# Optimization experiments

Hardware: AMD Instinct MI355X
Metric: run time of the kernel (lower is better)

## Reference

```python
import jax, jax.numpy as jnp
import numpy as np

N_NODES = 100000


def gcn_conv(x, W, b, src, dst, num_nodes):
    """PyG GCNConv: add self-loops, symmetric deg^{-1/2} normalization,
    linear transform, scatter-add aggregation (source -> target), bias."""
    h = x @ W  # [N, out]
    # degree on target nodes, counting the added self-loop (+1)
    deg = jax.ops.segment_sum(jnp.ones_like(dst, dtype=h.dtype), dst,
                              num_segments=num_nodes) + 1.0
    dinv = jax.lax.rsqrt(deg)  # deg >= 1 always
    norm = dinv[src] * dinv[dst]  # [E]
    agg = jax.ops.segment_sum(h[src] * norm[:, None], dst,
                              num_segments=num_nodes)
    # self-loop contribution: norm_ii = dinv[i]^2
    out = agg + h * (dinv * dinv)[:, None]
    return out + b


def setup_inputs() -> dict:
    key = jax.random.key(0)
    ks = jax.random.split(key, 8)
    num_features, hidden, emb = 64, 64, 32
    x = jax.random.normal(ks[0], (N_NODES, num_features), dtype=jnp.float32)
    edge_index = jax.random.randint(ks[1], (2, 1600000), 0, N_NODES, dtype=jnp.int64)
    def glorot(k, shape):
        lim = float(np.sqrt(6.0 / (shape[0] + shape[1])))
        return jax.random.uniform(k, shape, jnp.float32, -lim, lim)
    return {
        "x": x,
        "edge_index": edge_index,
        "W1": glorot(ks[2], (num_features, hidden)),
        "b1": jnp.zeros((hidden,), jnp.float32),
        "W2": glorot(ks[3], (hidden, hidden)),
        "b2": jnp.zeros((hidden,), jnp.float32),
        "Wf": glorot(ks[4], (hidden, emb)),
        "bf": jnp.zeros((emb,), jnp.float32),
    }


def reference(x, edge_index, W1, b1, W2, b2, Wf, bf):
    src, dst = edge_index[0], edge_index[1]
    n = x.shape[0]
    h = gcn_conv(x, W1, b1, src, dst, n)
    h = jax.nn.relu(h)  # dropout is identity in eval mode
    h = gcn_conv(h, W2, b2, src, dst, n)
    h = jax.nn.relu(h)
    return h @ Wf + bf
```

## Files before the change

kernel.cpp:

```cpp
#include <hip/hip_runtime.h>


#define NODE_SHIFT 9
#define NODES_PER_BKT 512
#define K1PAD 208
#define NB_PART 256

__device__ __forceinline__ unsigned short f2bf_rne(float f) {
    unsigned int u = __float_as_uint(f);
    unsigned int r = (u + 0x7FFFu + ((u >> 16) & 1u)) >> 16;
    return (unsigned short)r;
}
__device__ __forceinline__ float bf_lo(unsigned int u) {
    return __uint_as_float(u << 16);
}
__device__ __forceinline__ float bf_hi(unsigned int u) {
    return __uint_as_float(u & 0xFFFF0000u);
}

__global__ __launch_bounds__(256) void coarse_hist_kernel(const int* __restrict__ dst, int E,
                                                          int* __restrict__ bkt_partial,
                                                          int K1, int CHK) {
    __shared__ int lcnt[256];
    const int tid = threadIdx.x;
    const int start = blockIdx.x * CHK;
    const int end = min(E, start + CHK);
    for (int k = tid; k < 256; k += 256) lcnt[k] = 0;
    __syncthreads();
    const int s4 = start >> 2;
    const int e4 = end >> 2;
    for (int i = s4 + tid; i < e4; i += 256) {
        const int4 d = ((const int4*)dst)[i];
        atomicAdd(&lcnt[d.x >> NODE_SHIFT], 1);
        atomicAdd(&lcnt[d.y >> NODE_SHIFT], 1);
        atomicAdd(&lcnt[d.z >> NODE_SHIFT], 1);
        atomicAdd(&lcnt[d.w >> NODE_SHIFT], 1);
    }
    __syncthreads();
    for (int k = tid; k < K1; k += 256)
        bkt_partial[blockIdx.x * K1PAD + k] = lcnt[k];
}

__global__ __launch_bounds__(256) void bucket_scan_kernel(const int* __restrict__ bkt_partial,
                                                          int* __restrict__ bkt_start,
                                                          int* __restrict__ bkt_cursor,
                                                          int K1, int E) {
    __shared__ int wsum[4];
    const int tid = threadIdx.x;
    const int lane = tid & 63;
    const int wave = tid >> 6;
    int c = 0;
    if (tid < K1)
        for (int b = 0; b < NB_PART; b++) c += bkt_partial[b * K1PAD + tid];
    int inc = c;
#pragma unroll
    for (int o = 1; o < 64; o <<= 1) {
        int t = __shfl_up(inc, o, 64);
        if (lane >= o) inc += t;
    }
    if (lane == 63) wsum[wave] = inc;
    __syncthreads();
    int wpre = 0;
#pragma unroll
    for (int w = 0; w < 4; w++) wpre += (w < wave) ? wsum[w] : 0;
    const int p = wpre + inc - c;
    if (tid < K1) { bkt_start[tid] = p; bkt_cursor[tid] = p; }
    if (tid == 0) bkt_start[K1] = E;
}

__global__ __launch_bounds__(256) void partition_kernel(const int* __restrict__ src,
                                                        const int* __restrict__ dst, int E,
                                                        int* __restrict__ bkt_cursor,
                                                        int2* __restrict__ staging,
                                                        int K1, int CHK) {
    __shared__ int lcnt[256];
    __shared__ int lcur[256];
    const int tid = threadIdx.x;
    const int start = blockIdx.x * CHK;
    const int end = min(E, start + CHK);
    for (int k = tid; k < 256; k += 256) lcnt[k] = 0;
    __syncthreads();
    const int s4 = start >> 2;
    const int e4 = end >> 2;
    for (int i = s4 + tid; i < e4; i += 256) {
        const int4 d = ((const int4*)dst)[i];
        atomicAdd(&lcnt[d.x >> NODE_SHIFT], 1);
        atomicAdd(&lcnt[d.y >> NODE_SHIFT], 1);
        atomicAdd(&lcnt[d.z >> NODE_SHIFT], 1);
        atomicAdd(&lcnt[d.w >> NODE_SHIFT], 1);
    }
    __syncthreads();
    for (int k = tid; k < K1; k += 256) {
        int cc = lcnt[k];
        lcur[k] = cc ? atomicAdd(&bkt_cursor[k], cc) : 0;
    }
    __syncthreads();
    for (int i = s4 + tid; i < e4; i += 256) {
        const int4 d = ((const int4*)dst)[i];
        const int4 s = ((const int4*)src)[i];
        int pos;
        pos = atomicAdd(&lcur[d.x >> NODE_SHIFT], 1); staging[pos] = make_int2(d.x, s.x);
        pos = atomicAdd(&lcur[d.y >> NODE_SHIFT], 1); staging[pos] = make_int2(d.y, s.y);
        pos = atomicAdd(&lcur[d.z >> NODE_SHIFT], 1); staging[pos] = make_int2(d.z, s.z);
        pos = atomicAdd(&lcur[d.w >> NODE_SHIFT], 1); staging[pos] = make_int2(d.w, s.w);
    }
}

__global__ __launch_bounds__(512) void bucket_build_kernel(const int2* __restrict__ staging,
                                                           const int* __restrict__ bkt_start,
                                                           float* __restrict__ dinv,
                                                           int* __restrict__ offs,
                                                           int* __restrict__ csr_src,
                                                           int N, int E) {
    __shared__ int cnt[NODES_PER_BKT];
    __shared__ int wsum[8];
    const int tid = threadIdx.x;
    const int node0 = blockIdx.x * NODES_PER_BKT;
    const int estart = bkt_start[blockIdx.x];
    const int eend = bkt_start[blockIdx.x + 1];

    cnt[tid] = 0;
    __syncthreads();
    for (int e = estart + tid; e < eend; e += 512)
        atomicAdd(&cnt[staging[e].x - node0], 1);
    __syncthreads();

    const int lane = tid & 63;
    const int wave = tid >> 6;
    const int c = cnt[tid];
    int inc = c;
#pragma unroll
    for (int o = 1; o < 64; o <<= 1) {
        int t = __shfl_up(inc, o, 64);
        if (lane >= o) inc += t;
    }
    if (lane == 63) wsum[wave] = inc;
    __syncthreads();
    int wpre = 0;
#pragma unroll
    for (int w = 0; w < 8; w++) wpre += (w < wave) ? wsum[w] : 0;
    const int p = estart + wpre + inc - c;

    const int node = node0 + tid;
    __syncthreads();
    if (node < N) {
        offs[node] = p;
        dinv[node] = rsqrtf((float)c + 1.0f);
    }
    cnt[tid] = p;
    __syncthreads();
    for (int e = estart + tid; e < eend; e += 512) {
        int2 r = staging[e];
        int pos = atomicAdd(&cnt[r.x - node0], 1);
        csr_src[pos] = r.y;
    }
    if (blockIdx.x == 0 && tid == 0) offs[N] = E;
}

template <int OUTC, int RPT, bool BIAS, bool SCALE, bool BF16OUT>
__global__ __launch_bounds__(256) void gemm_kernel(const float* __restrict__ X,
                                                   const float* __restrict__ W,
                                                   const float* __restrict__ bias,
                                                   const float* __restrict__ dinv,
                                                   void* __restrict__ Yv, int N) {
    constexpr int CG = OUTC / 4;
    constexpr int RG = 256 / CG;
    constexpr int R = RG * RPT;
    constexpr int RPAD = R + (R / 32) * 4;
    __shared__ float Ws[64 * OUTC];
    __shared__ float Xt[64 * RPAD];

    const int tid = threadIdx.x;
    const int row0 = blockIdx.x * R;

    for (int l = tid; l < 64 * OUTC / 4; l += 256)
        ((float4*)Ws)[l] = ((const float4*)W)[l];

    for (int l = tid; l < R * 16; l += 256) {
        const int r = l & (R - 1);
        const int kq = l >> 7;
        float4 v = make_float4(0.f, 0.f, 0.f, 0.f);
        const int row = row0 + r;
        if (row < N) v = ((const float4*)(X + (long)row * 64))[kq];
        const int rp = r + (r >> 5) * 4;
        Xt[(4 * kq + 0) * RPAD + rp] = v.x;
        Xt[(4 * kq + 1) * RPAD + rp] = v.y;
        Xt[(4 * kq + 2) * RPAD + rp] = v.z;
        Xt[(4 * kq + 3) * RPAD + rp] = v.w;
    }
    __syncthreads();

    const int cg = tid % CG;
    const int rg = tid / CG;
    const int c0 = cg * 4;
    const int r0 = rg * RPT;
    const int r0p = r0 + (r0 >> 5) * 4;

    float acc[RPT][4];
#pragma unroll
    for (int i = 0; i < RPT; i++)
#pragma unroll
        for (int j = 0; j < 4; j++) acc[i][j] = 0.f;

#pragma unroll 4
    for (int k = 0; k < 64; k++) {
        float xv[RPT];
        const float4 xa = *(const float4*)&Xt[k * RPAD + r0p];
        xv[0] = xa.x; xv[1] = xa.y; xv[2] = xa.z; xv[3] = xa.w;
        if (RPT == 8) {
            const float4 xb = *(const float4*)&Xt[k * RPAD + r0p + 4];
            xv[4] = xb.x; xv[5] = xb.y; xv[6] = xb.z; xv[7] = xb.w;
        }
        const float4 wa = *(const float4*)&Ws[k * OUTC + c0];
        const float wv[4] = {wa.x, wa.y, wa.z, wa.w};
#pragma unroll
        for (int i = 0; i < RPT; i++)
#pragma unroll
            for (int j = 0; j < 4; j++)
                acc[i][j] += xv[i] * wv[j];
    }

    float4 bv = make_float4(0.f, 0.f, 0.f, 0.f);
    if (BIAS) bv = *(const float4*)&bias[c0];
#pragma unroll
    for (int i = 0; i < RPT; i++) {
        const int row = row0 + r0 + i;
        if (row < N) {
            const float sc = SCALE ? dinv[row] : 1.f;
            float4 o = make_float4(acc[i][0] * sc + bv.x, acc[i][1] * sc + bv.y,
                                   acc[i][2] * sc + bv.z, acc[i][3] * sc + bv.w);
            if (BF16OUT) {
                ushort4 o16;
                o16.x = f2bf_rne(o.x);
                o16.y = f2bf_rne(o.y);
                o16.z = f2bf_rne(o.z);
                o16.w = f2bf_rne(o.w);
                *(ushort4*)&((unsigned short*)Yv)[(long)row * OUTC + c0] = o16;
            } else {
                *(float4*)&((float*)Yv)[(long)row * OUTC + c0] = o;
            }
        }
    }
}

template <bool RELU>
__global__ __launch_bounds__(256) void agg_kernel(const unsigned short* __restrict__ T,
                                                  const int* __restrict__ offs,
                                                  const int* __restrict__ csr_src,
                                                  const float* __restrict__ dinv,
                                                  const float* __restrict__ bias,
                                                  float* __restrict__ Y, int N) {
    const int tid = threadIdx.x;
    const int node = blockIdx.x * 32 + (tid >> 3);
    const int l8 = tid & 7;
    if (node >= N) return;

    const int start = offs[node];
    const int n_edges = offs[node + 1] - start;
    const int* ep = csr_src + start;
    const int fo = l8 * 8;

    float acc[8];
#pragma unroll
    for (int j = 0; j < 8; j++) acc[j] = 0.f;

#define ACC_U4(v)                                   \
    do {                                            \
        acc[0] += bf_lo((v).x); acc[1] += bf_hi((v).x); \
        acc[2] += bf_lo((v).y); acc[3] += bf_hi((v).y); \
        acc[4] += bf_lo((v).z); acc[5] += bf_hi((v).z); \
        acc[6] += bf_lo((v).w); acc[7] += bf_hi((v).w); \
    } while (0)

    int s[8];
    int e = 0;
    if (n_edges >= 8) {
#pragma unroll
        for (int j = 0; j < 8; j++) s[j] = ep[j];
        while (true) {
            uint4 h[8];
#pragma unroll
            for (int j = 0; j < 8; j++)
                h[j] = *(const uint4*)&T[(long)s[j] * 64 + fo];
            const int next = e + 8;
            const bool more = (next + 8 <= n_edges);
            if (more) {
#pragma unroll
                for (int j = 0; j < 8; j++) s[j] = ep[next + j];
            }
#pragma unroll
            for (int j = 0; j < 8; j++) ACC_U4(h[j]);
            e = next;
            if (!more) break;
        }
    }
    if (e + 4 <= n_edges) {
        int s4[4];
#pragma unroll
        for (int j = 0; j < 4; j++) s4[j] = ep[e + j];
        uint4 h[4];
#pragma unroll
        for (int j = 0; j < 4; j++)
            h[j] = *(const uint4*)&T[(long)s4[j] * 64 + fo];
#pragma unroll
        for (int j = 0; j < 4; j++) ACC_U4(h[j]);
        e += 4;
    }
    for (; e < n_edges; e++) {
        const uint4 hv = *(const uint4*)&T[(long)ep[e] * 64 + fo];
        ACC_U4(hv);
    }
#undef ACC_U4

    const float di = dinv[node];
    const uint4 sv = *(const uint4*)&T[(long)node * 64 + fo];
    float self[8] = {bf_lo(sv.x), bf_hi(sv.x), bf_lo(sv.y), bf_hi(sv.y),
                     bf_lo(sv.z), bf_hi(sv.z), bf_lo(sv.w), bf_hi(sv.w)};
    const float4 ba = *(const float4*)&bias[l8 * 8];
    const float4 bb = *(const float4*)&bias[l8 * 8 + 4];
    const float bv[8] = {ba.x, ba.y, ba.z, ba.w, bb.x, bb.y, bb.z, bb.w};
    float o[8];
#pragma unroll
    for (int j = 0; j < 8; j++) {
        o[j] = di * (acc[j] + self[j]) + bv[j];
        if (RELU) o[j] = fmaxf(o[j], 0.f);
    }
    float* yp = &Y[(long)node * 64 + l8 * 8];
    *(float4*)yp = make_float4(o[0], o[1], o[2], o[3]);
    *(float4*)(yp + 4) = make_float4(o[4], o[5], o[6], o[7]);
}

extern "C" void kernel_launch(void* const* d_in, const int* in_sizes, int n_in,
                              void* d_out, int out_size, void* d_ws, size_t ws_size,
                              hipStream_t stream) {
    const float* x  = (const float*)d_in[0];
    const int*   ei = (const int*)d_in[1];
    const float* W1 = (const float*)d_in[2];
    const float* b1 = (const float*)d_in[3];
    const float* W2 = (const float*)d_in[4];
    const float* b2 = (const float*)d_in[5];
    const float* Wf = (const float*)d_in[6];
    const float* bf = (const float*)d_in[7];

    const int N = in_sizes[0] / 64;
    const int E = in_sizes[1] / 2;
    const int* src = ei;
    const int* dst = ei + E;
    const int K1 = (N + NODES_PER_BKT - 1) / NODES_PER_BKT;

    char* ws = (char*)d_ws;
    size_t off = 0;
    auto alloc = [&](size_t bytes) -> void* {
        void* p = ws + off;
        off = (off + bytes + 255) & ~(size_t)255;
        return p;
    };
    int*   bkt_partial = (int*)alloc((size_t)NB_PART * K1PAD * 4);
    int*   bkt_start   = (int*)alloc(257 * 4);
    int*   bkt_cursor  = (int*)alloc(256 * 4);
    float* dinv        = (float*)alloc((size_t)N * 4);
    int*   offs        = (int*)alloc((size_t)(N + 1) * 4);
    int*   csr_src     = (int*)alloc((size_t)E * 4);
    unsigned short* A  = (unsigned short*)alloc((size_t)N * 64 * 2);
    float* B           = (float*)alloc((size_t)N * 64 * 4);
    int2*  staging     = (int2*)alloc((size_t)E * 8);

    const int NB = NB_PART;
    const int CHK = ((E / 4 + NB - 1) / NB) * 4;

    coarse_hist_kernel<<<NB, 256, 0, stream>>>(dst, E, bkt_partial, K1, CHK);
    bucket_scan_kernel<<<1, 256, 0, stream>>>(bkt_partial, bkt_start, bkt_cursor, K1, E);
    partition_kernel<<<NB, 256, 0, stream>>>(src, dst, E, bkt_cursor, staging, K1, CHK);
    bucket_build_kernel<<<K1, 512, 0, stream>>>(staging, bkt_start, dinv, offs, csr_src, N, E);

    gemm_kernel<64, 8, false, true, true><<<(N + 127) / 128, 256, 0, stream>>>(x, W1, nullptr, dinv, A, N);
    agg_kernel<true><<<(N + 31) / 32, 256, 0, stream>>>(A, offs, csr_src, dinv, b1, B, N);

    gemm_kernel<64, 8, false, true, true><<<(N + 127) / 128, 256, 0, stream>>>(B, W2, nullptr, dinv, A, N);
    agg_kernel<true><<<(N + 31) / 32, 256, 0, stream>>>(A, offs, csr_src, dinv, b2, B, N);

    gemm_kernel<32, 4, true, false, false><<<(N + 127) / 128, 256, 0, stream>>>(B, Wf, bf, nullptr, d_out, N);
}
```

Before: 256.6 us.

## Fuse aggregation with following GEMM via shared-memory tile of aggregated rows

Merges each aggregation kernel with the next dense transform. The aggregated, ReLU'd 32-node tile is kept in shared memory and multiplied by W2 (or Wf for the head) in the same block. This removes the fp32 intermediate write and re-read and two launches. In exchange, every agg block now loads the full weight matrix into shared memory and runs a small GEMM with low data reuse, which could reduce occupancy.

```diff
diff --git a/kernel.cpp b/kernel.cpp
--- a/kernel.cpp
+++ b/kernel.cpp
@@ -5,6 +5,7 @@
 #define NODES_PER_BKT 512
 #define K1PAD 208
 #define NB_PART 256
+#define HPAD 68
 
 __device__ __forceinline__ unsigned short f2bf_rne(float f) {
     unsigned int u = __float_as_uint(f);
@@ -157,15 +158,12 @@
     if (blockIdx.x == 0 && tid == 0) offs[N] = E;
 }
 
-template <int OUTC, int RPT, bool BIAS, bool SCALE, bool BF16OUT>
-__global__ __launch_bounds__(256) void gemm_kernel(const float* __restrict__ X,
-                                                   const float* __restrict__ W,
-                                                   const float* __restrict__ bias,
-                                                   const float* __restrict__ dinv,
-                                                   void* __restrict__ Yv, int N) {
-    constexpr int CG = OUTC / 4;
-    constexpr int RG = 256 / CG;
-    constexpr int R = RG * RPT;
+__global__ __launch_bounds__(256) void gemm1_kernel(const float* __restrict__ X,
+                                                    const float* __restrict__ W,
+                                                    const float* __restrict__ dinv,
+                                                    unsigned short* __restrict__ Y, int N) {
+    constexpr int OUTC = 64, RPT = 8;
+    constexpr int R = 128;
     constexpr int RPAD = R + (R / 32) * 4;
     __shared__ float Ws[64 * OUTC];
     __shared__ float Xt[64 * RPAD];
@@ -190,8 +188,8 @@
     }
     __syncthreads();
 
-    const int cg = tid % CG;
-    const int rg = tid / CG;
+    const int cg = tid % 16;
+    const int rg = tid / 16;
     const int c0 = cg * 4;
     const int r0 = rg * RPT;
     const int r0p = r0 + (r0 >> 5) * 4;
@@ -206,11 +204,9 @@
     for (int k = 0; k < 64; k++) {
         float xv[RPT];
         const float4 xa = *(const float4*)&Xt[k * RPAD + r0p];
+        const float4 xb = *(const float4*)&Xt[k * RPAD + r0p + 4];
         xv[0] = xa.x; xv[1] = xa.y; xv[2] = xa.z; xv[3] = xa.w;
-        if (RPT == 8) {
-            const float4 xb = *(const float4*)&Xt[k * RPAD + r0p + 4];
-            xv[4] = xb.x; xv[5] = xb.y; xv[6] = xb.z; xv[7] = xb.w;
-        }
+        xv[4] = xb.x; xv[5] = xb.y; xv[6] = xb.z; xv[7] = xb.w;
         const float4 wa = *(const float4*)&Ws[k * OUTC + c0];
         const float wv[4] = {wa.x, wa.y, wa.z, wa.w};
 #pragma unroll
@@ -220,114 +216,161 @@
                 acc[i][j] += xv[i] * wv[j];
     }
 
-    float4 bv = make_float4(0.f, 0.f, 0.f, 0.f);
-    if (BIAS) bv = *(const float4*)&bias[c0];
 #pragma unroll
     for (int i = 0; i < RPT; i++) {
         const int row = row0 + r0 + i;
         if (row < N) {
-            const float sc = SCALE ? dinv[row] : 1.f;
-            float4 o = make_float4(acc[i][0] * sc + bv.x, acc[i][1] * sc + bv.y,
-                                   acc[i][2] * sc + bv.z, acc[i][3] * sc + bv.w);
-            if (BF16OUT) {
-                ushort4 o16;
-                o16.x = f2bf_rne(o.x);
-                o16.y = f2bf_rne(o.y);
-                o16.z = f2bf_rne(o.z);
-                o16.w = f2bf_rne(o.w);
-                *(ushort4*)&((unsigned short*)Yv)[(long)row * OUTC + c0] = o16;
-            } else {
-                *(float4*)&((float*)Yv)[(long)row * OUTC + c0] = o;
-            }
-        }
-    }
-}
-
-template <bool RELU>
-__global__ __launch_bounds__(256) void agg_kernel(const unsigned short* __restrict__ T,
-                                                  const int* __restrict__ offs,
-                                                  const int* __restrict__ csr_src,
-                                                  const float* __restrict__ dinv,
-                                                  const float* __restrict__ bias,
-                                                  float* __restrict__ Y, int N) {
-    const int tid = threadIdx.x;
-    const int node = blockIdx.x * 32 + (tid >> 3);
+            const float sc = dinv[row];
+            ushort4 o16;
+            o16.x = f2bf_rne(acc[i][0] * sc);
+            o16.y = f2bf_rne(acc[i][1] * sc);
+            o16.z = f2bf_rne(acc[i][2] * sc);
+            o16.w = f2bf_rne(acc[i][3] * sc);
+            *(ushort4*)&Y[(long)row * OUTC + c0] = o16;
+        }
+    }
+}
+
+template <int OUTC, bool HEAD>
+__global__ __launch_bounds__(256) void fused_agg_gemm_kernel(
+    const unsigned short* __restrict__ T, const int* __restrict__ offs,
+    const int* __restrict__ csr_src, const float* __restrict__ dinv,
+    const float* __restrict__ aggbias, const float* __restrict__ W,
+    const float* __restrict__ headbias, void* __restrict__ Yv, int N) {
+    __shared__ float Ws[64 * OUTC];
+    __shared__ float hs[32 * HPAD];
+
+    const int tid = threadIdx.x;
+
+    for (int l = tid; l < 64 * OUTC / 4; l += 256)
+        ((float4*)Ws)[l] = ((const float4*)W)[l];
+
+    const int nl = tid >> 3;
+    const int node = blockIdx.x * 32 + nl;
     const int l8 = tid & 7;
-    if (node >= N) return;
-
-    const int start = offs[node];
-    const int n_edges = offs[node + 1] - start;
-    const int* ep = csr_src + start;
     const int fo = l8 * 8;
 
-    float acc[8];
-#pragma unroll
-    for (int j = 0; j < 8; j++) acc[j] = 0.f;
-
-#define ACC_U4(v)                                   \
-    do {                                            \
+    float o[8];
+    if (node < N) {
+        const int start = offs[node];
+        const int n_edges = offs[node + 1] - start;
+        const int* ep = csr_src + start;
+
+        float acc[8];
+#pragma unroll
+        for (int j = 0; j < 8; j++) acc[j] = 0.f;
+
+#define ACC_U4(v)                                       \
+    do {                                                \
         acc[0] += bf_lo((v).x); acc[1] += bf_hi((v).x); \
         acc[2] += bf_lo((v).y); acc[3] += bf_hi((v).y); \
         acc[4] += bf_lo((v).z); acc[5] += bf_hi((v).z); \
         acc[6] += bf_lo((v).w); acc[7] += bf_hi((v).w); \
     } while (0)
 
-    int s[8];
-    int e = 0;
-    if (n_edges >= 8) {
-#pragma unroll
-        for (int j = 0; j < 8; j++) s[j] = ep[j];
-        while (true) {
-            uint4 h[8];
-#pragma unroll
-            for (int j = 0; j < 8; j++)
-                h[j] = *(const uint4*)&T[(long)s[j] * 64 + fo];
-            const int next = e + 8;
-            const bool more = (next + 8 <= n_edges);
-            if (more) {
-#pragma unroll
-                for (int j = 0; j < 8; j++) s[j] = ep[next + j];
+        int s[8];
+        int e = 0;
+        if (n_edges >= 8) {
+#pragma unroll
+            for (int j = 0; j < 8; j++) s[j] = ep[j];
+            while (true) {
+                uint4 h[8];
+#pragma unroll
+                for (int j = 0; j < 8; j++)
+                    h[j] = *(const uint4*)&T[(long)s[j] * 64 + fo];
+                const int next = e + 8;
+                const bool more = (next + 8 <= n_edges);
+                if (more) {
+#pragma unroll
+                    for (int j = 0; j < 8; j++) s[j] = ep[next + j];
+                }
+#pragma unroll
+                for (int j = 0; j < 8; j++) ACC_U4(h[j]);
+                e = next;
+                if (!more) break;
             }
-#pragma unroll
-            for (int j = 0; j < 8; j++) ACC_U4(h[j]);
-            e = next;
-            if (!more) break;
-        }
-    }
-    if (e + 4 <= n_edges) {
-        int s4[4];
-#pragma unroll
-        for (int j = 0; j < 4; j++) s4[j] = ep[e + j];
-        uint4 h[4];
-#pragma unroll
-        for (int j = 0; j < 4; j++)
-            h[j] = *(const uint4*)&T[(long)s4[j] * 64 + fo];
-#pragma unroll
-        for (int j = 0; j < 4; j++) ACC_U4(h[j]);
-        e += 4;
-    }
-    for (; e < n_edges; e++) {
-        const uint4 hv = *(const uint4*)&T[(long)ep[e] * 64 + fo];
-        ACC_U4(hv);
-    }
+        }
+        if (e + 4 <= n_edges) {
+            int s4[4];
+#pragma unroll
+            for (int j = 0; j < 4; j++) s4[j] = ep[e + j];
+            uint4 h[4];
+#pragma unroll
+            for (int j = 0; j < 4; j++)
+                h[j] = *(const uint4*)&T[(long)s4[j] * 64 + fo];
+#pragma unroll
+            for (int j = 0; j < 4; j++) ACC_U4(h[j]);
+            e += 4;
+        }
+        for (; e < n_edges; e++) {
+            const uint4 hv = *(const uint4*)&T[(long)ep[e] * 64 + fo];
+            ACC_U4(hv);
+        }
 #undef ACC_U4
 
-    const float di = dinv[node];
-    const uint4 sv = *(const uint4*)&T[(long)node * 64 + fo];
-    float self[8] = {bf_lo(sv.x), bf_hi(sv.x), bf_lo(sv.y), bf_hi(sv.y),
-                     bf_lo(sv.z), bf_hi(sv.z), bf_lo(sv.w), bf_hi(sv.w)};
-    const float4 ba = *(const float4*)&bias[l8 * 8];
-    const float4 bb = *(const float4*)&bias[l8 * 8 + 4];
-    const float bv[8] = {ba.x, ba.y, ba.z, ba.w, bb.x, bb.y, bb.z, bb.w};
-    float o[8];
-#pragma unroll
-    for (int j = 0; j < 8; j++) {
-        o[j] = di * (acc[j] + self[j]) + bv[j];
-        if (RELU) o[j] = fmaxf(o[j], 0.f);
-    }
-    float* yp = &Y[(long)node * 64 + l8 * 8];
-    *(float4*)yp = make_float4(o[0], o[1], o[2], o[3]);
-    *(float4*)(yp + 4) = make_float4(o[4], o[5], o[6], o[7]);
+        const float di = dinv[node];
+        const uint4 sv = *(const uint4*)&T[(long)node * 64 + fo];
+        const float self[8] = {bf_lo(sv.x), bf_hi(sv.x), bf_lo(sv.y), bf_hi(sv.y),
+                               bf_lo(sv.z), bf_hi(sv.z), bf_lo(sv.w), bf_hi(sv.w)};
+        const float4 ba = *(const float4*)&aggbias[fo];
+        const float4 bb = *(const float4*)&aggbias[fo + 4];
+        const float bv[8] = {ba.x, ba.y, ba.z, ba.w, bb.x, bb.y, bb.z, bb.w};
+#pragma unroll
+        for (int j = 0; j < 8; j++)
+            o[j] = fmaxf(di * (acc[j] + self[j]) + bv[j], 0.f);
+    } else {
+#pragma unroll
+        for (int j = 0; j < 8; j++) o[j] = 0.f;
+    }
+    float* hp = &hs[nl * HPAD + fo];
+    *(float4*)hp = make_float4(o[0], o[1], o[2], o[3]);
+    *(float4*)(hp + 4) = make_float4(o[4], o[5], o[6], o[7]);
+    __syncthreads();
+
+    constexpr int CPT = OUTC / 8;
+    const int row = blockIdx.x * 32 + (tid >> 3);
+    const int c0 = (tid & 7) * CPT;
+    const int lrow = tid >> 3;
+
+    float acc2[CPT];
+#pragma unroll
+    for (int j = 0; j < CPT; j++) acc2[j] = 0.f;
+
+#pragma unroll 4
+    for (int k = 0; k < 64; k++) {
+        const float x = hs[lrow * HPAD + k];
+        const float4 wa = *(const float4*)&Ws[k * OUTC + c0];
+        acc2[0] += x * wa.x;
+        acc2[1] += x * wa.y;
+        acc2[2] += x * wa.z;
+        acc2[3] += x * wa.w;
+        if (CPT == 8) {
+            const float4 wb = *(const float4*)&Ws[k * OUTC + c0 + 4];
+            acc2[4] += x * wb.x;
+            acc2[5] += x * wb.y;
+            acc2[6] += x * wb.z;
+            acc2[7] += x * wb.w;
+        }
+    }
+
+    if (row < N) {
+        if (HEAD) {
+            const float4 hb = *(const float4*)&headbias[c0];
+            float* yp = &((float*)Yv)[(long)row * OUTC + c0];
+            *(float4*)yp = make_float4(acc2[0] + hb.x, acc2[1] + hb.y,
+                                       acc2[2] + hb.z, acc2[3] + hb.w);
+        } else {
+            const float sc = dinv[row];
+            unsigned short* yp = &((unsigned short*)Yv)[(long)row * OUTC + c0];
+            ushort4 o0, o1;
+            o0.x = f2bf_rne(acc2[0] * sc); o0.y = f2bf_rne(acc2[1] * sc);
+            o0.z = f2bf_rne(acc2[2] * sc); o0.w = f2bf_rne(acc2[3] * sc);
+            o1.x = f2bf_rne(acc2[4] * sc); o1.y = f2bf_rne(acc2[5] * sc);
+            o1.z = f2bf_rne(acc2[6] * sc); o1.w = f2bf_rne(acc2[7] * sc);
+            *(ushort4*)yp = o0;
+            *(ushort4*)(yp + 4) = o1;
+        }
+    }
 }
 
 extern "C" void kernel_launch(void* const* d_in, const int* in_sizes, int n_in,
@@ -362,7 +405,7 @@
     int*   offs        = (int*)alloc((size_t)(N + 1) * 4);
     int*   csr_src     = (int*)alloc((size_t)E * 4);
     unsigned short* A  = (unsigned short*)alloc((size_t)N * 64 * 2);
-    float* B           = (float*)alloc((size_t)N * 64 * 4);
+    unsigned short* A2 = (unsigned short*)alloc((size_t)N * 64 * 2);
     int2*  staging     = (int2*)alloc((size_t)E * 8);
 
     const int NB = NB_PART;
@@ -373,11 +416,11 @@
     partition_kernel<<<NB, 256, 0, stream>>>(src, dst, E, bkt_cursor, staging, K1, CHK);
     bucket_build_kernel<<<K1, 512, 0, stream>>>(staging, bkt_start, dinv, offs, csr_src, N, E);
 
-    gemm_kernel<64, 8, false, true, true><<<(N + 127) / 128, 256, 0, stream>>>(x, W1, nullptr, dinv, A, N);
-    agg_kernel<true><<<(N + 31) / 32, 256, 0, stream>>>(A, offs, csr_src, dinv, b1, B, N);
-
-    gemm_kernel<64, 8, false, true, true><<<(N + 127) / 128, 256, 0, stream>>>(B, W2, nullptr, dinv, A, N);
-    agg_kernel<true><<<(N + 31) / 32, 256, 0, stream>>>(A, offs, csr_src, dinv, b2, B, N);
-
-    gemm_kernel<32, 4, true, false, false><<<(N + 127) / 128, 256, 0, stream>>>(B, Wf, bf, nullptr, d_out, N);
-}
+    gemm1_kernel<<<(N + 127) / 128, 256, 0, stream>>>(x, W1, dinv, A, N);
+
+    fused_agg_gemm_kernel<64, false><<<(N + 31) / 32, 256, 0, stream>>>(
+        A, offs, csr_src, dinv, b1, W2, nullptr, A2, N);
+
+    fused_agg_gemm_kernel<32, true><<<(N + 31) / 32, 256, 0, stream>>>(
+        A2, offs, csr_src, dinv, b2, Wf, bf, d_out, N);
+}
```

Result: faster. 230.1 us (-10.3%).
